# Optimization experiments

Hardware: AMD Instinct MI355X
Metric: run time of the kernel (lower is better)

Reference implementation:

```python
import jax, jax.numpy as jnp
import numpy as np


def setup_inputs() -> dict:
    key = jax.random.key(0)
    k1, k2, k3 = jax.random.split(key, 3)
    B, N, D = 8, 4096, 64
    q = jax.random.normal(k1, (B, N, D), dtype=jnp.float32)
    k = jax.random.normal(k2, (B, N, D), dtype=jnp.float32)
    v = jax.random.normal(k3, (B, N, D), dtype=jnp.float32)
    attn_mask = jnp.ones((B, N), dtype=jnp.int32)  # 1 = attend, 0 = padding
    return {"q": q, "k": k, "v": v, "attn_mask": attn_mask}


def reference(q, k, v, attn_mask):
    # q: [B, n_q, d], k/v: [B, n_k, d], attn_mask: [B, n_k]
    d = q.shape[-1]
    n_q, n_k = q.shape[1], k.shape[1]
    scale = jnp.sqrt(jnp.asarray(d, dtype=q.dtype))
    # [B, n_q, n_k] attention logits
    logits = jnp.einsum("bqd,bkd->bqk", q, k) / scale
    # causal (mask_future=True): tril keep-mask over (n_q, n_k)
    causal = jnp.tril(jnp.ones((n_q, n_k), dtype=bool))
    neg_inf = jnp.asarray(-jnp.inf, dtype=logits.dtype)
    logits = jnp.where(causal[None, :, :], logits, neg_inf)
    # padding mask broadcast over query dim: [B, 1, n_k]
    logits = jnp.where(attn_mask[:, None, :] == 0, neg_inf, logits)
    w = jax.nn.softmax(logits, axis=-1)
    return jnp.einsum("bqk,bkd->bqd", w, v)
```

## Files before the change

### kernel.cpp

```cpp
#include <hip/hip_runtime.h>


#define BATCH 8
#define SEQ   4096
#define DIM   64
#define QT    64
#define NKT   (SEQ / 64)

typedef __attribute__((ext_vector_type(8))) short bf16x8;
typedef __attribute__((ext_vector_type(4))) float f32x4;

__device__ inline short f2bf(float f) {
    unsigned u = __builtin_bit_cast(unsigned, f);
    u += 0x7FFFu + ((u >> 16) & 1u);
    return (short)(u >> 16);
}

__device__ inline unsigned pk2bf(float a, float b) {
    unsigned ua = __builtin_bit_cast(unsigned, a) + 0x8000u;
    unsigned ub = __builtin_bit_cast(unsigned, b) + 0x8000u;
    return __builtin_amdgcn_perm(ub, ua, 0x07060302u);
}

__device__ inline float fast_exp2(float x) {
#if __has_builtin(__builtin_amdgcn_exp2f)
    return __builtin_amdgcn_exp2f(x);
#else
    return exp2f(x);
#endif
}

__device__ inline void gl_lds16(const void* g, void* l) {
    __builtin_amdgcn_global_load_lds(
        (const __attribute__((address_space(1))) void*)g,
        (__attribute__((address_space(3))) void*)l, 16, 0, 0);
}

__global__ __launch_bounds__(256)
void prep_kv(const float* __restrict__ kg, const float* __restrict__ vg,
             const int* __restrict__ mg, short* __restrict__ kw,
             short* __restrict__ vw, float* __restrict__ mf) {
    const int tile = blockIdx.x;
    const float* kp = kg + (size_t)tile * 64 * DIM;
    const float* vp = vg + (size_t)tile * 64 * DIM;
    short* ko = kw + (size_t)tile * 4096;
    short* vo = vw + (size_t)tile * 4096;
    const int t = threadIdx.x;
    if (mf && t < 64) {
        const int* mp = mg + (size_t)tile * 64;
        mf[(size_t)tile * 64 + t] = mp[t] ? 0.0f : -1e30f;
    }
#pragma unroll
    for (int i = 0; i < 4; ++i) {
        const int flat = i * 256 + t;
        const int key = flat >> 4, d0 = (flat & 15) * 4;
        const float4 kv = *(const float4*)(kp + (size_t)key * DIM + d0);
        uint2 kpk;
        kpk.x = pk2bf(kv.x, kv.y); kpk.y = pk2bf(kv.z, kv.w);
        *(uint2*)(ko + (((d0 >> 3) << 6) + key) * 8 + (d0 & 7)) = kpk;
        const float4 vv = *(const float4*)(vp + (size_t)key * DIM + d0);
        const int kc = key >> 3, jk = key & 7;
        vo[((kc << 6) + d0 + 0) * 8 + jk] = f2bf(vv.x);
        vo[((kc << 6) + d0 + 1) * 8 + jk] = f2bf(vv.y);
        vo[((kc << 6) + d0 + 2) * 8 + jk] = f2bf(vv.z);
        vo[((kc << 6) + d0 + 3) * 8 + jk] = f2bf(vv.w);
    }
}

__global__ __launch_bounds__(512, 6)
void attn_split3(const float* __restrict__ qg, float* __restrict__ og,
                 const short* __restrict__ kw, const short* __restrict__ vw,
                 const float* __restrict__ mf, float* __restrict__ opart,
                 float* __restrict__ lpart) {
    __shared__ __align__(16) char smem[43008];
    short* KbS = (short*)smem;
    short* VbS = (short*)(smem + 16384);
    short* PbS = (short*)(smem + 32768);
    float* OX = (float*)smem;
    float* LB = (float*)(smem + 16384);

    const int t    = threadIdx.x;
    const int w    = t >> 6;
    const int L    = t & 63;
    const int c15  = L & 15;
    const int quad = L >> 4;
    const int qsub = w & 3;
    const int kh   = w >> 2;

    const int id  = blockIdx.x;
    const int b   = id & 7;
    const int r_  = id >> 3;
    const int j   = r_ & 31;
    const int ch  = r_ >> 5;
    const int nL  = 64 - j;
    const int qLt = 63 - j;

    const float* qp  = qg + (size_t)b * SEQ * DIM;
    const float* mb  = mf + (size_t)b * SEQ;
    const short* kwb = kw + (size_t)b * NKT * 4096;
    const short* vwb = vw + (size_t)b * NKT * 4096;
    float* osl = opart + (size_t)(b * 32 + j) * 8192;
    float* lsl = lpart + (size_t)(b * 32 + j) * 256;
    const float qscale = 0.125f * 1.44269504088896340736f;

    auto stage = [&](int bs, int kt) {
        const short* ks = kwb + (size_t)kt * 4096;
        const short* vs = vwb + (size_t)kt * 4096;
        const int off = w << 9;
        gl_lds16(ks + off + (L << 3), KbS + bs * 4096 + off);
        gl_lds16(vs + off + (L << 3), VbS + bs * 4096 + off);
    };

    short* Pw = PbS + w * 640;

    int sqt[2], sk0[2], sk1[2], smode[2], sos[2], sls[2], nseg;
    sos[0] = sos[1] = 0; sls[0] = sls[1] = 0;
    if (ch == 0) {
        nseg = 1;
        sqt[0] = qLt; sk0[0] = 0;  sk1[0] = 22; smode[0] = 0; sls[0] = 0;
    } else if (ch == 1) {
        if (nL >= 44) {
            nseg = 1;
            sqt[0] = qLt; sk0[0] = 22; sk1[0] = 44; smode[0] = 1; sos[0] = 0; sls[0] = 1;
        } else {
            nseg = 2;
            sqt[0] = qLt; sk0[0] = 22; sk1[0] = nL;      smode[0] = 1; sos[0] = 0; sls[0] = 1;
            sqt[1] = j;   sk0[1] = 0;  sk1[1] = 44 - nL; smode[1] = 0; sls[1] = 3;
        }
    } else {
        if (nL > 44) {
            nseg = 2;
            sqt[0] = qLt; sk0[0] = 44; sk1[0] = nL;    smode[0] = 1; sos[0] = 1; sls[0] = 2;
            sqt[1] = j;   sk0[1] = 0;  sk1[1] = j + 1; smode[1] = 2;
        } else if (nL == 44) {
            nseg = 1;
            sqt[0] = j; sk0[0] = 0; sk1[0] = j + 1; smode[0] = 2;
        } else {
            nseg = 1;
            sqt[0] = j; sk0[0] = 44 - nL; sk1[0] = j + 1; smode[0] = 1; sos[0] = 1; sls[0] = 2;
        }
    }

    for (int seg = 0; seg < nseg; ++seg) {
        const int qt   = sqt[seg];
        const int kt0  = sk0[seg];
        const int kt1  = sk1[seg];
        const int mode = smode[seg];

        const int qbase = qt * QT;
        const int qrow  = qbase + qsub * 16 + c15;

        bf16x8 Qf[2];
#pragma unroll
        for (int c = 0; c < 2; ++c) {
            const float* src = qp + (size_t)qrow * DIM + c * 32 + quad * 8;
            float4 x = *(const float4*)(src);
            float4 y = *(const float4*)(src + 4);
            bf16x8 f;
            f[0] = f2bf(x.x * qscale); f[1] = f2bf(x.y * qscale);
            f[2] = f2bf(x.z * qscale); f[3] = f2bf(x.w * qscale);
            f[4] = f2bf(y.x * qscale); f[5] = f2bf(y.y * qscale);
            f[6] = f2bf(y.z * qscale); f[7] = f2bf(y.w * qscale);
            Qf[c] = f;
        }

        float lsum = 0.0f;
        f32x4 Oacc[4];
#pragma unroll
        for (int nb = 0; nb < 4; ++nb) Oacc[nb] = (f32x4){0.f, 0.f, 0.f, 0.f};

        stage(0, kt0);

        for (int kt = kt0; kt < kt1; ++kt) {
            const int cur = (kt - kt0) & 1;
            __syncthreads();
            if (kt + 1 < kt1) stage(cur ^ 1, kt + 1);

            const short* Kt = KbS + cur * 4096;
            const short* Vt = VbS + cur * 4096;

            f32x4 sacc[2];
            sacc[0] = (f32x4){0.f, 0.f, 0.f, 0.f};
            sacc[1] = (f32x4){0.f, 0.f, 0.f, 0.f};
#pragma unroll
            for (int c = 0; c < 2; ++c) {
#pragma unroll
                for (int i = 0; i < 2; ++i) {
                    bf16x8 kf = *(const bf16x8*)&Kt[(((quad + 4 * c) << 6) + (2 * kh + i) * 16 + c15) * 8];
                    sacc[i] = __builtin_amdgcn_mfma_f32_16x16x32_bf16(kf, Qf[c], sacc[i], 0, 0, 0);
                }
            }

            const bool diag = (kt == qt);
#pragma unroll
            for (int i = 0; i < 2; ++i) {
                const int kb = 2 * kh + i;
                const float4 ma = *(const float4*)&mb[kt * 64 + kb * 16 + quad * 4];
                const float mar[4] = {ma.x, ma.y, ma.z, ma.w};
                float p[4];
#pragma unroll
                for (int r = 0; r < 4; ++r) {
                    float s = sacc[i][r] + mar[r];
                    if (diag) {
                        const int keyg = kt * 64 + kb * 16 + quad * 4 + r;
                        if (keyg > qrow) s = -1e30f;
                    }
                    p[r] = fast_exp2(fminf(s, 80.0f));
                    lsum += p[r];
                }
                uint2 pp;
                pp.x = pk2bf(p[0], p[1]);
                pp.y = pk2bf(p[2], p[3]);
                *(uint2*)&Pw[c15 * 40 + i * 16 + quad * 4] = pp;
            }

            bf16x8 pf = *(const bf16x8*)&Pw[c15 * 40 + quad * 8];
#pragma unroll
            for (int nb = 0; nb < 4; ++nb) {
                bf16x8 vf = *(const bf16x8*)&Vt[(((kh * 4 + quad) << 6) + nb * 16 + c15) * 8];
                Oacc[nb] = __builtin_amdgcn_mfma_f32_16x16x32_bf16(pf, vf, Oacc[nb], 0, 0, 0);
            }
        }

        lsum += __shfl_xor(lsum, 16);
        lsum += __shfl_xor(lsum, 32);

        __syncthreads();
        if (w >= 4) {
            const int g = w & 3;
#pragma unroll
            for (int r = 0; r < 4; ++r) {
                const int q = quad * 4 + r;
#pragma unroll
                for (int nb = 0; nb < 4; ++nb)
                    OX[(g * 16 + q) * 64 + nb * 16 + c15] = Oacc[nb][r];
            }
            if (quad == 0) LB[g * 16 + c15] = lsum;
        }
        __syncthreads();
        if (w < 4) {
            const float ltot = lsum + LB[w * 16 + c15];
            const float inv  = 1.0f / ltot;
            float* dst = (mode == 1) ? osl + (size_t)sos[seg] * 4096
                                     : og + ((size_t)b * SEQ + qbase) * DIM;
            if (mode != 2 && L < 16)
                lsl[sls[seg] * 64 + w * 16 + L] = ltot;
#pragma unroll
            for (int r = 0; r < 4; ++r) {
                const float ir = (mode == 2)
                    ? __shfl(inv, (L & 48) + ((L & 48) >> 2) + r) : 1.0f;
                const int rl = w * 16 + quad * 4 + r;
#pragma unroll
                for (int nb = 0; nb < 4; ++nb)
                    dst[(size_t)rl * DIM + nb * 16 + c15] =
                        (Oacc[nb][r] + OX[rl * 64 + nb * 16 + c15]) * ir;
            }
        }
        __syncthreads();
    }
}

__global__ __launch_bounds__(256)
void merge3(float* __restrict__ og, const float* __restrict__ opart,
            const float* __restrict__ lpart) {
    const int id = blockIdx.x;
    const int b = id & 7, j = id >> 3;
    const int nL = 64 - j, qLt = 63 - j;
    const float* os = opart + (size_t)(b * 32 + j) * 8192;
    const float* ls = lpart + (size_t)(b * 32 + j) * 256;
    const int t = threadIdx.x;
    const bool hasC = (nL > 44);

    float* opL = og + ((size_t)b * SEQ + (size_t)qLt * 64) * DIM;
#pragma unroll
    for (int i = 0; i < 4; ++i) {
        const int flat = i * 256 + t;
        const int row = flat >> 4;
        const int c4  = (flat & 15) * 4;
        float l = ls[row] + ls[64 + row];
        if (hasC) l += ls[128 + row];
        const float inv = 1.0f / l;
        const float4 a  = *(const float4*)(opL + (size_t)row * DIM + c4);
        const float4 p0 = *(const float4*)(os + (size_t)row * 64 + c4);
        float4 r;
        if (hasC) {
            const float4 p1 = *(const float4*)(os + 4096 + (size_t)row * 64 + c4);
            r.x = (a.x + p0.x + p1.x) * inv;
            r.y = (a.y + p0.y + p1.y) * inv;
            r.z = (a.z + p0.z + p1.z) * inv;
            r.w = (a.w + p0.w + p1.w) * inv;
        } else {
            r.x = (a.x + p0.x) * inv;
            r.y = (a.y + p0.y) * inv;
            r.z = (a.z + p0.z) * inv;
            r.w = (a.w + p0.w) * inv;
        }
        *(float4*)(opL + (size_t)row * DIM + c4) = r;
    }

    if (nL < 44) {
        float* opS = og + ((size_t)b * SEQ + (size_t)j * 64) * DIM;
#pragma unroll
        for (int i = 0; i < 4; ++i) {
            const int flat = i * 256 + t;
            const int row = flat >> 4;
            const int c4  = (flat & 15) * 4;
            const float inv = 1.0f / (ls[192 + row] + ls[128 + row]);
            const float4 a  = *(const float4*)(opS + (size_t)row * DIM + c4);
            const float4 p1 = *(const float4*)(os + 4096 + (size_t)row * 64 + c4);
            float4 r;
            r.x = (a.x + p1.x) * inv;
            r.y = (a.y + p1.y) * inv;
            r.z = (a.z + p1.z) * inv;
            r.w = (a.w + p1.w) * inv;
            *(float4*)(opS + (size_t)row * DIM + c4) = r;
        }
    }
}

template <bool WS>
__global__ __launch_bounds__(512, 4)
void attn_fwd(const float* __restrict__ qg, const float* __restrict__ kg,
              const float* __restrict__ vg, const int* __restrict__ mg,
              float* __restrict__ og, const short* __restrict__ kw,
              const short* __restrict__ vw) {
    __shared__ __align__(16) char smem[59392];
    short* KbS = (short*)smem;
    short* VbS = (short*)(smem + 16384);
    short* PbS = (short*)(smem + 32768);
    float* Ml  = (float*)(smem + 43008);
    float* OX = (float*)smem;
    float* LB = (float*)(smem + 16384);

    const int t    = threadIdx.x;
    const int w    = t >> 6;
    const int L    = t & 63;
    const int c15  = L & 15;
    const int quad = L >> 4;
    const int qsub = w & 3;
    const int kh   = w >> 2;

    const int id = blockIdx.x;
    const int b  = id & 7;
    const int j  = id >> 3;
    const int qb = (j < 32) ? (63 - j) : (j - 32);
    const int qbase  = qb * QT;
    const int ntiles = qb + 1;

    const float* qp = qg + (size_t)b * SEQ * DIM;
    const float* kp = kg + (size_t)b * SEQ * DIM;
    const float* vp = vg + (size_t)b * SEQ * DIM;
    const int*   mp = mg + (size_t)b * SEQ;
    const short* kwb = WS ? kw + (size_t)b * NKT * 4096 : nullptr;
    const short* vwb = WS ? vw + (size_t)b * NKT * 4096 : nullptr;

    const int qrow = qbase + qsub * 16 + c15;
    const float qscale = 0.125f * 1.44269504088896340736f;

    bf16x8 Qf[2];
#pragma unroll
    for (int c = 0; c < 2; ++c) {
        const float* src = qp + (size_t)qrow * DIM + c * 32 + quad * 8;
        float4 x = *(const float4*)(src);
        float4 y = *(const float4*)(src + 4);
        bf16x8 f;
        f[0] = f2bf(x.x * qscale); f[1] = f2bf(x.y * qscale);
        f[2] = f2bf(x.z * qscale); f[3] = f2bf(x.w * qscale);
        f[4] = f2bf(y.x * qscale); f[5] = f2bf(y.y * qscale);
        f[6] = f2bf(y.z * qscale); f[7] = f2bf(y.w * qscale);
        Qf[c] = f;
    }

    auto stage = [&](int bs, int kt) {
        const short* ks = kwb + (size_t)kt * 4096;
        const short* vs = vwb + (size_t)kt * 4096;
        const int off = w << 9;
        gl_lds16(ks + off + (L << 3), KbS + bs * 4096 + off);
        gl_lds16(vs + off + (L << 3), VbS + bs * 4096 + off);
    };

    for (int i = t; i < ntiles * 64; i += 512)
        Ml[i] = mp[i] ? 0.0f : -1e30f;

    float lsum = 0.0f;
    f32x4 Oacc[4];
#pragma unroll
    for (int nb = 0; nb < 4; ++nb) Oacc[nb] = (f32x4){0.f, 0.f, 0.f, 0.f};

    if constexpr (WS) stage(0, 0);

    short* Pw = PbS + w * 640;

    for (int kt = 0; kt < ntiles; ++kt) {
        const int cur = WS ? (kt & 1) : 0;

        if constexpr (!WS) {
            __syncthreads();
#pragma unroll
            for (int it = 0; it < 2; ++it) {
                const int flat = it * 512 + t;
                const int key = flat >> 4, d0 = (flat & 15) * 4;
                const float4 kv = *(const float4*)(kp + (size_t)(kt * 64 + key) * DIM + d0);
                uint2 kk;
                kk.x = pk2bf(kv.x, kv.y); kk.y = pk2bf(kv.z, kv.w);
                *(uint2*)&KbS[(((d0 >> 3) << 6) + key) * 8 + (d0 & 7)] = kk;
                const float4 vv = *(const float4*)(vp + (size_t)(kt * 64 + key) * DIM + d0);
                const int kc = key >> 3, jk = key & 7;
                VbS[((kc << 6) + d0 + 0) * 8 + jk] = f2bf(vv.x);
                VbS[((kc << 6) + d0 + 1) * 8 + jk] = f2bf(vv.y);
                VbS[((kc << 6) + d0 + 2) * 8 + jk] = f2bf(vv.z);
                VbS[((kc << 6) + d0 + 3) * 8 + jk] = f2bf(vv.w);
            }
            __syncthreads();
        } else {
            __syncthreads();
            if (kt + 1 < ntiles) stage(cur ^ 1, kt + 1);
        }

        const short* Kt = KbS + cur * 4096;
        const short* Vt = VbS + cur * 4096;

        f32x4 sacc[2];
        sacc[0] = (f32x4){0.f, 0.f, 0.f, 0.f};
        sacc[1] = (f32x4){0.f, 0.f, 0.f, 0.f};
#pragma unroll
        for (int c = 0; c < 2; ++c) {
#pragma unroll
            for (int i = 0; i < 2; ++i) {
                bf16x8 kf = *(const bf16x8*)&Kt[(((quad + 4 * c) << 6) + (2 * kh + i) * 16 + c15) * 8];
                sacc[i] = __builtin_amdgcn_mfma_f32_16x16x32_bf16(kf, Qf[c], sacc[i], 0, 0, 0);
            }
        }

        const bool diag = (kt == ntiles - 1);
#pragma unroll
        for (int i = 0; i < 2; ++i) {
            const int kb = 2 * kh + i;
            const float4 ma = *(const float4*)&Ml[kt * 64 + kb * 16 + quad * 4];
            const float mar[4] = {ma.x, ma.y, ma.z, ma.w};
            float p[4];
#pragma unroll
            for (int r = 0; r < 4; ++r) {
                float s = sacc[i][r] + mar[r];
                if (diag) {
                    const int keyg = kt * 64 + kb * 16 + quad * 4 + r;
                    if (keyg > qrow) s = -1e30f;
                }
                p[r] = fast_exp2(fminf(s, 80.0f));
                lsum += p[r];
            }
            uint2 pp;
            pp.x = pk2bf(p[0], p[1]);
            pp.y = pk2bf(p[2], p[3]);
            *(uint2*)&Pw[c15 * 40 + i * 16 + quad * 4] = pp;
        }

        bf16x8 pf = *(const bf16x8*)&Pw[c15 * 40 + quad * 8];
#pragma unroll
        for (int nb = 0; nb < 4; ++nb) {
            bf16x8 vf = *(const bf16x8*)&Vt[(((kh * 4 + quad) << 6) + nb * 16 + c15) * 8];
            Oacc[nb] = __builtin_amdgcn_mfma_f32_16x16x32_bf16(pf, vf, Oacc[nb], 0, 0, 0);
        }
    }

    lsum += __shfl_xor(lsum, 16);
    lsum += __shfl_xor(lsum, 32);

    __syncthreads();
    if (w >= 4) {
        const int g = w & 3;
#pragma unroll
        for (int r = 0; r < 4; ++r) {
            const int q = quad * 4 + r;
#pragma unroll
            for (int nb = 0; nb < 4; ++nb)
                OX[(g * 16 + q) * 64 + nb * 16 + c15] = Oacc[nb][r];
        }
        if (quad == 0) LB[g * 16 + c15] = lsum;
    }
    __syncthreads();
    if (w < 4) {
        const float inv = 1.0f / (lsum + LB[w * 16 + c15]);
        float* op = og + (size_t)b * SEQ * DIM;
#pragma unroll
        for (int r = 0; r < 4; ++r) {
            const float ir = __shfl(inv, (L & 48) + ((L & 48) >> 2) + r);
            const int row = qbase + w * 16 + quad * 4 + r;
#pragma unroll
            for (int nb = 0; nb < 4; ++nb)
                op[(size_t)row * DIM + nb * 16 + c15] =
                    (Oacc[nb][r] + OX[(w * 16 + quad * 4 + r) * 64 + nb * 16 + c15]) * ir;
        }
    }
}

extern "C" void kernel_launch(void* const* d_in, const int* in_sizes, int n_in,
                              void* d_out, int out_size, void* d_ws, size_t ws_size,
                              hipStream_t stream) {
    (void)in_sizes; (void)n_in; (void)out_size;
    const float* q = (const float*)d_in[0];
    const float* k = (const float*)d_in[1];
    const float* v = (const float*)d_in[2];
    const int*   m = (const int*)d_in[3];
    float* o = (float*)d_out;

    const size_t kvB    = (size_t)BATCH * NKT * 4096 * sizeof(short);
    const size_t maddB  = (size_t)BATCH * SEQ * sizeof(float);
    const size_t opartB = (size_t)BATCH * 32 * 8192 * sizeof(float);
    const size_t lpartB = (size_t)BATCH * 32 * 256 * sizeof(float);
    const size_t need3  = 2 * kvB + maddB + opartB + lpartB;

    if (ws_size >= need3) {
        short* kw = (short*)d_ws;
        short* vw = kw + (size_t)BATCH * NKT * 4096;
        float* mf = (float*)((char*)d_ws + 2 * kvB);
        float* opart = (float*)((char*)d_ws + 2 * kvB + maddB);
        float* lpart = opart + (size_t)BATCH * 32 * 8192;
        prep_kv<<<dim3(BATCH * NKT), 256, 0, stream>>>(k, v, m, kw, vw, mf);
        attn_split3<<<dim3(768), 512, 0, stream>>>(q, o, kw, vw, mf, opart, lpart);
        merge3<<<dim3(256), 256, 0, stream>>>(o, opart, lpart);
    } else if (ws_size >= 2 * kvB) {
        short* kw = (short*)d_ws;
        short* vw = kw + (size_t)BATCH * NKT * 4096;
        prep_kv<<<dim3(BATCH * NKT), 256, 0, stream>>>(k, v, m, kw, vw, nullptr);
        attn_fwd<true><<<dim3(512), 512, 0, stream>>>(q, k, v, m, o, kw, vw);
    } else {
        attn_fwd<false><<<dim3(512), 512, 0, stream>>>(q, k, v, m, o, nullptr, nullptr);
    }
}
```

Before: 124.0 us.

## Split causal attention into four chunks and keep P in registers

Result: slower. 131.3 us (+5.9%).

```diff
diff --git a/kernel.cpp b/kernel.cpp
--- a/kernel.cpp
+++ b/kernel.cpp
@@ -9,6 +9,7 @@
 
 typedef __attribute__((ext_vector_type(8))) short bf16x8;
 typedef __attribute__((ext_vector_type(4))) float f32x4;
+typedef __attribute__((ext_vector_type(4))) unsigned u32x4;
 
 __device__ inline short f2bf(float f) {
     unsigned u = __builtin_bit_cast(unsigned, f);
@@ -59,23 +60,23 @@
         kpk.x = pk2bf(kv.x, kv.y); kpk.y = pk2bf(kv.z, kv.w);
         *(uint2*)(ko + (((d0 >> 3) << 6) + key) * 8 + (d0 & 7)) = kpk;
         const float4 vv = *(const float4*)(vp + (size_t)key * DIM + d0);
-        const int kc = key >> 3, jk = key & 7;
-        vo[((kc << 6) + d0 + 0) * 8 + jk] = f2bf(vv.x);
-        vo[((kc << 6) + d0 + 1) * 8 + jk] = f2bf(vv.y);
-        vo[((kc << 6) + d0 + 2) * 8 + jk] = f2bf(vv.z);
-        vo[((kc << 6) + d0 + 3) * 8 + jk] = f2bf(vv.w);
-    }
-}
-
-__global__ __launch_bounds__(512, 6)
-void attn_split3(const float* __restrict__ qg, float* __restrict__ og,
+        const int vcell = ((key >> 5) << 2) | ((key >> 2) & 3);
+        const int vj    = (((key >> 4) & 1) << 2) | (key & 3);
+        vo[((vcell << 6) + d0 + 0) * 8 + vj] = f2bf(vv.x);
+        vo[((vcell << 6) + d0 + 1) * 8 + vj] = f2bf(vv.y);
+        vo[((vcell << 6) + d0 + 2) * 8 + vj] = f2bf(vv.z);
+        vo[((vcell << 6) + d0 + 3) * 8 + vj] = f2bf(vv.w);
+    }
+}
+
+__global__ __launch_bounds__(512, 8)
+void attn_split4(const float* __restrict__ qg, float* __restrict__ og,
                  const short* __restrict__ kw, const short* __restrict__ vw,
                  const float* __restrict__ mf, float* __restrict__ opart,
                  float* __restrict__ lpart) {
-    __shared__ __align__(16) char smem[43008];
+    __shared__ __align__(16) char smem[32768];
     short* KbS = (short*)smem;
     short* VbS = (short*)(smem + 16384);
-    short* PbS = (short*)(smem + 32768);
     float* OX = (float*)smem;
     float* LB = (float*)(smem + 16384);
 
@@ -99,8 +100,8 @@
     const float* mb  = mf + (size_t)b * SEQ;
     const short* kwb = kw + (size_t)b * NKT * 4096;
     const short* vwb = vw + (size_t)b * NKT * 4096;
-    float* osl = opart + (size_t)(b * 32 + j) * 8192;
-    float* lsl = lpart + (size_t)(b * 32 + j) * 256;
+    float* osl = opart + (size_t)(b * 32 + j) * 12288;
+    float* lsl = lpart + (size_t)(b * 32 + j) * 384;
     const float qscale = 0.125f * 1.44269504088896340736f;
 
     auto stage = [&](int bs, int kt) {
@@ -111,33 +112,34 @@
         gl_lds16(vs + off + (L << 3), VbS + bs * 4096 + off);
     };
 
-    short* Pw = PbS + w * 640;
-
     int sqt[2], sk0[2], sk1[2], smode[2], sos[2], sls[2], nseg;
     sos[0] = sos[1] = 0; sls[0] = sls[1] = 0;
     if (ch == 0) {
         nseg = 1;
-        sqt[0] = qLt; sk0[0] = 0;  sk1[0] = 22; smode[0] = 0; sls[0] = 0;
+        sqt[0] = qLt; sk0[0] = 0;  sk1[0] = 16; smode[0] = 0; sls[0] = 0;
     } else if (ch == 1) {
-        if (nL >= 44) {
+        nseg = 1;
+        sqt[0] = qLt; sk0[0] = 16; sk1[0] = 32; smode[0] = 1; sos[0] = 0; sls[0] = 1;
+    } else if (ch == 2) {
+        if (nL >= 48) {
             nseg = 1;
-            sqt[0] = qLt; sk0[0] = 22; sk1[0] = 44; smode[0] = 1; sos[0] = 0; sls[0] = 1;
+            sqt[0] = qLt; sk0[0] = 32; sk1[0] = 48; smode[0] = 1; sos[0] = 1; sls[0] = 2;
         } else {
             nseg = 2;
-            sqt[0] = qLt; sk0[0] = 22; sk1[0] = nL;      smode[0] = 1; sos[0] = 0; sls[0] = 1;
-            sqt[1] = j;   sk0[1] = 0;  sk1[1] = 44 - nL; smode[1] = 0; sls[1] = 3;
+            sqt[0] = qLt; sk0[0] = 32; sk1[0] = nL;      smode[0] = 1; sos[0] = 1; sls[0] = 2;
+            sqt[1] = j;   sk0[1] = 0;  sk1[1] = 48 - nL; smode[1] = 0; sls[1] = 4;
         }
     } else {
-        if (nL > 44) {
+        if (nL > 48) {
             nseg = 2;
-            sqt[0] = qLt; sk0[0] = 44; sk1[0] = nL;    smode[0] = 1; sos[0] = 1; sls[0] = 2;
+            sqt[0] = qLt; sk0[0] = 48; sk1[0] = nL;    smode[0] = 1; sos[0] = 2; sls[0] = 3;
             sqt[1] = j;   sk0[1] = 0;  sk1[1] = j + 1; smode[1] = 2;
-        } else if (nL == 44) {
+        } else if (nL == 48) {
             nseg = 1;
             sqt[0] = j; sk0[0] = 0; sk1[0] = j + 1; smode[0] = 2;
         } else {
             nseg = 1;
-            sqt[0] = j; sk0[0] = 44 - nL; sk1[0] = j + 1; smode[0] = 1; sos[0] = 1; sls[0] = 2;
+            sqt[0] = j; sk0[0] = 48 - nL; sk1[0] = j + 1; smode[0] = 1; sos[0] = 2; sls[0] = 5;
         }
     }
 
@@ -192,6 +194,7 @@
             }
 
             const bool diag = (kt == qt);
+            unsigned pu[4];
 #pragma unroll
             for (int i = 0; i < 2; ++i) {
                 const int kb = 2 * kh + i;
@@ -208,13 +211,12 @@
                     p[r] = fast_exp2(fminf(s, 80.0f));
                     lsum += p[r];
                 }
-                uint2 pp;
-                pp.x = pk2bf(p[0], p[1]);
-                pp.y = pk2bf(p[2], p[3]);
-                *(uint2*)&Pw[c15 * 40 + i * 16 + quad * 4] = pp;
-            }
-
-            bf16x8 pf = *(const bf16x8*)&Pw[c15 * 40 + quad * 8];
+                pu[2 * i]     = pk2bf(p[0], p[1]);
+                pu[2 * i + 1] = pk2bf(p[2], p[3]);
+            }
+
+            const bf16x8 pf = __builtin_bit_cast(bf16x8,
+                (u32x4){pu[0], pu[1], pu[2], pu[3]});
 #pragma unroll
             for (int nb = 0; nb < 4; ++nb) {
                 bf16x8 vf = *(const bf16x8*)&Vt[(((kh * 4 + quad) << 6) + nb * 16 + c15) * 8];
@@ -261,15 +263,15 @@
 }
 
 __global__ __launch_bounds__(256)
-void merge3(float* __restrict__ og, const float* __restrict__ opart,
+void merge4(float* __restrict__ og, const float* __restrict__ opart,
             const float* __restrict__ lpart) {
     const int id = blockIdx.x;
     const int b = id & 7, j = id >> 3;
     const int nL = 64 - j, qLt = 63 - j;
-    const float* os = opart + (size_t)(b * 32 + j) * 8192;
-    const float* ls = lpart + (size_t)(b * 32 + j) * 256;
+    const float* os = opart + (size_t)(b * 32 + j) * 12288;
+    const float* ls = lpart + (size_t)(b * 32 + j) * 384;
     const int t = threadIdx.x;
-    const bool hasC = (nL > 44);
+    const bool has3 = (nL > 48);
 
     float* opL = og + ((size_t)b * SEQ + (size_t)qLt * 64) * DIM;
 #pragma unroll
@@ -277,42 +279,40 @@
         const int flat = i * 256 + t;
         const int row = flat >> 4;
         const int c4  = (flat & 15) * 4;
-        float l = ls[row] + ls[64 + row];
-        if (hasC) l += ls[128 + row];
+        float l = ls[row] + ls[64 + row] + ls[128 + row];
+        if (has3) l += ls[192 + row];
         const float inv = 1.0f / l;
         const float4 a  = *(const float4*)(opL + (size_t)row * DIM + c4);
         const float4 p0 = *(const float4*)(os + (size_t)row * 64 + c4);
+        const float4 p1 = *(const float4*)(os + 4096 + (size_t)row * 64 + c4);
+        float sx = a.x + p0.x + p1.x;
+        float sy = a.y + p0.y + p1.y;
+        float sz = a.z + p0.z + p1.z;
+        float sw = a.w + p0.w + p1.w;
+        if (has3) {
+            const float4 p2 = *(const float4*)(os + 8192 + (size_t)row * 64 + c4);
+            sx += p2.x; sy += p2.y; sz += p2.z; sw += p2.w;
+        }
         float4 r;
-        if (hasC) {
-            const float4 p1 = *(const float4*)(os + 4096 + (size_t)row * 64 + c4);
-            r.x = (a.x + p0.x + p1.x) * inv;
-            r.y = (a.y + p0.y + p1.y) * inv;
-            r.z = (a.z + p0.z + p1.z) * inv;
-            r.w = (a.w + p0.w + p1.w) * inv;
-        } else {
-            r.x = (a.x + p0.x) * inv;
-            r.y = (a.y + p0.y) * inv;
-            r.z = (a.z + p0.z) * inv;
-            r.w = (a.w + p0.w) * inv;
-        }
+        r.x = sx * inv; r.y = sy * inv; r.z = sz * inv; r.w = sw * inv;
         *(float4*)(opL + (size_t)row * DIM + c4) = r;
     }
 
-    if (nL < 44) {
+    if (nL < 48) {
         float* opS = og + ((size_t)b * SEQ + (size_t)j * 64) * DIM;
 #pragma unroll
         for (int i = 0; i < 4; ++i) {
             const int flat = i * 256 + t;
             const int row = flat >> 4;
             const int c4  = (flat & 15) * 4;
-            const float inv = 1.0f / (ls[192 + row] + ls[128 + row]);
+            const float inv = 1.0f / (ls[256 + row] + ls[320 + row]);
             const float4 a  = *(const float4*)(opS + (size_t)row * DIM + c4);
-            const float4 p1 = *(const float4*)(os + 4096 + (size_t)row * 64 + c4);
+            const float4 p2 = *(const float4*)(os + 8192 + (size_t)row * 64 + c4);
             float4 r;
-            r.x = (a.x + p1.x) * inv;
-            r.y = (a.y + p1.y) * inv;
-            r.z = (a.z + p1.z) * inv;
-            r.w = (a.w + p1.w) * inv;
+            r.x = (a.x + p2.x) * inv;
+            r.y = (a.y + p2.y) * inv;
+            r.z = (a.z + p2.z) * inv;
+            r.w = (a.w + p2.w) * inv;
             *(float4*)(opS + (size_t)row * DIM + c4) = r;
         }
     }
@@ -327,7 +327,6 @@
     __shared__ __align__(16) char smem[59392];
     short* KbS = (short*)smem;
     short* VbS = (short*)(smem + 16384);
-    short* PbS = (short*)(smem + 32768);
     float* Ml  = (float*)(smem + 43008);
     float* OX = (float*)smem;
     float* LB = (float*)(smem + 16384);
@@ -389,8 +388,6 @@
 
     if constexpr (WS) stage(0, 0);
 
-    short* Pw = PbS + w * 640;
-
     for (int kt = 0; kt < ntiles; ++kt) {
         const int cur = WS ? (kt & 1) : 0;
 
@@ -405,11 +402,12 @@
                 kk.x = pk2bf(kv.x, kv.y); kk.y = pk2bf(kv.z, kv.w);
                 *(uint2*)&KbS[(((d0 >> 3) << 6) + key) * 8 + (d0 & 7)] = kk;
                 const float4 vv = *(const float4*)(vp + (size_t)(kt * 64 + key) * DIM + d0);
-                const int kc = key >> 3, jk = key & 7;
-                VbS[((kc << 6) + d0 + 0) * 8 + jk] = f2bf(vv.x);
-                VbS[((kc << 6) + d0 + 1) * 8 + jk] = f2bf(vv.y);
-                VbS[((kc << 6) + d0 + 2) * 8 + jk] = f2bf(vv.z);
-                VbS[((kc << 6) + d0 + 3) * 8 + jk] = f2bf(vv.w);
+                const int vcell = ((key >> 5) << 2) | ((key >> 2) & 3);
+                const int vj    = (((key >> 4) & 1) << 2) | (key & 3);
+                VbS[((vcell << 6) + d0 + 0) * 8 + vj] = f2bf(vv.x);
+                VbS[((vcell << 6) + d0 + 1) * 8 + vj] = f2bf(vv.y);
+                VbS[((vcell << 6) + d0 + 2) * 8 + vj] = f2bf(vv.z);
+                VbS[((vcell << 6) + d0 + 3) * 8 + vj] = f2bf(vv.w);
             }
             __syncthreads();
         } else {
@@ -433,6 +431,7 @@
         }
 
         const bool diag = (kt == ntiles - 1);
+        unsigned pu[4];
 #pragma unroll
         for (int i = 0; i < 2; ++i) {
             const int kb = 2 * kh + i;
@@ -449,13 +448,12 @@
                 p[r] = fast_exp2(fminf(s, 80.0f));
                 lsum += p[r];
             }
-            uint2 pp;
-            pp.x = pk2bf(p[0], p[1]);
-            pp.y = pk2bf(p[2], p[3]);
-            *(uint2*)&Pw[c15 * 40 + i * 16 + quad * 4] = pp;
-        }
-
-        bf16x8 pf = *(const bf16x8*)&Pw[c15 * 40 + quad * 8];
+            pu[2 * i]     = pk2bf(p[0], p[1]);
+            pu[2 * i + 1] = pk2bf(p[2], p[3]);
+        }
+
+        const bf16x8 pf = __builtin_bit_cast(bf16x8,
+            (u32x4){pu[0], pu[1], pu[2], pu[3]});
 #pragma unroll
         for (int nb = 0; nb < 4; ++nb) {
             bf16x8 vf = *(const bf16x8*)&Vt[(((kh * 4 + quad) << 6) + nb * 16 + c15) * 8];
@@ -506,19 +504,19 @@
 
     const size_t kvB    = (size_t)BATCH * NKT * 4096 * sizeof(short);
     const size_t maddB  = (size_t)BATCH * SEQ * sizeof(float);
-    const size_t opartB = (size_t)BATCH * 32 * 8192 * sizeof(float);
-    const size_t lpartB = (size_t)BATCH * 32 * 256 * sizeof(float);
-    const size_t need3  = 2 * kvB + maddB + opartB + lpartB;
-
-    if (ws_size >= need3) {
+    const size_t opartB = (size_t)BATCH * 32 * 12288 * sizeof(float);
+    const size_t lpartB = (size_t)BATCH * 32 * 384 * sizeof(float);
+    const size_t need4  = 2 * kvB + maddB + opartB + lpartB;
+
+    if (ws_size >= need4) {
         short* kw = (short*)d_ws;
         short* vw = kw + (size_t)BATCH * NKT * 4096;
         float* mf = (float*)((char*)d_ws + 2 * kvB);
         float* opart = (float*)((char*)d_ws + 2 * kvB + maddB);
-        float* lpart = opart + (size_t)BATCH * 32 * 8192;
+        float* lpart = opart + (size_t)BATCH * 32 * 12288;
         prep_kv<<<dim3(BATCH * NKT), 256, 0, stream>>>(k, v, m, kw, vw, mf);
-        attn_split3<<<dim3(768), 512, 0, stream>>>(q, o, kw, vw, mf, opart, lpart);
-        merge3<<<dim3(256), 256, 0, stream>>>(o, opart, lpart);
+        attn_split4<<<dim3(1024), 512, 0, stream>>>(q, o, kw, vw, mf, opart, lpart);
+        merge4<<<dim3(256), 256, 0, stream>>>(o, opart, lpart);
     } else if (ws_size >= 2 * kvB) {
         short* kw = (short*)d_ws;
         short* vw = kw + (size_t)BATCH * NKT * 4096;
```

## Keep softmax probabilities in registers by permuting V layout to match MFMA output

Applied to the files above, without the earlier changes.

New measurement: 124.9 us. Within noise of the previous version (+0.8%).

```diff
diff --git a/kernel.cpp b/kernel.cpp
--- a/kernel.cpp
+++ b/kernel.cpp
@@ -9,6 +9,7 @@
 
 typedef __attribute__((ext_vector_type(8))) short bf16x8;
 typedef __attribute__((ext_vector_type(4))) float f32x4;
+typedef __attribute__((ext_vector_type(4))) unsigned u32x4;
 
 __device__ inline short f2bf(float f) {
     unsigned u = __builtin_bit_cast(unsigned, f);
@@ -59,11 +60,12 @@
         kpk.x = pk2bf(kv.x, kv.y); kpk.y = pk2bf(kv.z, kv.w);
         *(uint2*)(ko + (((d0 >> 3) << 6) + key) * 8 + (d0 & 7)) = kpk;
         const float4 vv = *(const float4*)(vp + (size_t)key * DIM + d0);
-        const int kc = key >> 3, jk = key & 7;
-        vo[((kc << 6) + d0 + 0) * 8 + jk] = f2bf(vv.x);
-        vo[((kc << 6) + d0 + 1) * 8 + jk] = f2bf(vv.y);
-        vo[((kc << 6) + d0 + 2) * 8 + jk] = f2bf(vv.z);
-        vo[((kc << 6) + d0 + 3) * 8 + jk] = f2bf(vv.w);
+        const int vcell = ((key >> 5) << 2) | ((key >> 2) & 3);
+        const int vj    = (((key >> 4) & 1) << 2) | (key & 3);
+        vo[((vcell << 6) + d0 + 0) * 8 + vj] = f2bf(vv.x);
+        vo[((vcell << 6) + d0 + 1) * 8 + vj] = f2bf(vv.y);
+        vo[((vcell << 6) + d0 + 2) * 8 + vj] = f2bf(vv.z);
+        vo[((vcell << 6) + d0 + 3) * 8 + vj] = f2bf(vv.w);
     }
 }
 
@@ -72,10 +74,9 @@
                  const short* __restrict__ kw, const short* __restrict__ vw,
                  const float* __restrict__ mf, float* __restrict__ opart,
                  float* __restrict__ lpart) {
-    __shared__ __align__(16) char smem[43008];
+    __shared__ __align__(16) char smem[32768];
     short* KbS = (short*)smem;
     short* VbS = (short*)(smem + 16384);
-    short* PbS = (short*)(smem + 32768);
     float* OX = (float*)smem;
     float* LB = (float*)(smem + 16384);
 
@@ -110,8 +111,6 @@
         gl_lds16(ks + off + (L << 3), KbS + bs * 4096 + off);
         gl_lds16(vs + off + (L << 3), VbS + bs * 4096 + off);
     };
-
-    short* Pw = PbS + w * 640;
 
     int sqt[2], sk0[2], sk1[2], smode[2], sos[2], sls[2], nseg;
     sos[0] = sos[1] = 0; sls[0] = sls[1] = 0;
@@ -179,6 +178,9 @@
             const short* Kt = KbS + cur * 4096;
             const short* Vt = VbS + cur * 4096;
 
+            const float4 ma0 = *(const float4*)&mb[kt * 64 + (2 * kh + 0) * 16 + quad * 4];
+            const float4 ma1 = *(const float4*)&mb[kt * 64 + (2 * kh + 1) * 16 + quad * 4];
+
             f32x4 sacc[2];
             sacc[0] = (f32x4){0.f, 0.f, 0.f, 0.f};
             sacc[1] = (f32x4){0.f, 0.f, 0.f, 0.f};
@@ -192,10 +194,11 @@
             }
 
             const bool diag = (kt == qt);
+            unsigned pu[4];
 #pragma unroll
             for (int i = 0; i < 2; ++i) {
                 const int kb = 2 * kh + i;
-                const float4 ma = *(const float4*)&mb[kt * 64 + kb * 16 + quad * 4];
+                const float4 ma = i ? ma1 : ma0;
                 const float mar[4] = {ma.x, ma.y, ma.z, ma.w};
                 float p[4];
 #pragma unroll
@@ -208,13 +211,12 @@
                     p[r] = fast_exp2(fminf(s, 80.0f));
                     lsum += p[r];
                 }
-                uint2 pp;
-                pp.x = pk2bf(p[0], p[1]);
-                pp.y = pk2bf(p[2], p[3]);
-                *(uint2*)&Pw[c15 * 40 + i * 16 + quad * 4] = pp;
-            }
-
-            bf16x8 pf = *(const bf16x8*)&Pw[c15 * 40 + quad * 8];
+                pu[2 * i]     = pk2bf(p[0], p[1]);
+                pu[2 * i + 1] = pk2bf(p[2], p[3]);
+            }
+
+            const bf16x8 pf = __builtin_bit_cast(bf16x8,
+                (u32x4){pu[0], pu[1], pu[2], pu[3]});
 #pragma unroll
             for (int nb = 0; nb < 4; ++nb) {
                 bf16x8 vf = *(const bf16x8*)&Vt[(((kh * 4 + quad) << 6) + nb * 16 + c15) * 8];
@@ -327,7 +329,6 @@
     __shared__ __align__(16) char smem[59392];
     short* KbS = (short*)smem;
     short* VbS = (short*)(smem + 16384);
-    short* PbS = (short*)(smem + 32768);
     float* Ml  = (float*)(smem + 43008);
     float* OX = (float*)smem;
     float* LB = (float*)(smem + 16384);
@@ -389,8 +390,6 @@
 
     if constexpr (WS) stage(0, 0);
 
-    short* Pw = PbS + w * 640;
-
     for (int kt = 0; kt < ntiles; ++kt) {
         const int cur = WS ? (kt & 1) : 0;
 
@@ -405,11 +404,12 @@
                 kk.x = pk2bf(kv.x, kv.y); kk.y = pk2bf(kv.z, kv.w);
                 *(uint2*)&KbS[(((d0 >> 3) << 6) + key) * 8 + (d0 & 7)] = kk;
                 const float4 vv = *(const float4*)(vp + (size_t)(kt * 64 + key) * DIM + d0);
-                const int kc = key >> 3, jk = key & 7;
-                VbS[((kc << 6) + d0 + 0) * 8 + jk] = f2bf(vv.x);
-                VbS[((kc << 6) + d0 + 1) * 8 + jk] = f2bf(vv.y);
-                VbS[((kc << 6) + d0 + 2) * 8 + jk] = f2bf(vv.z);
-                VbS[((kc << 6) + d0 + 3) * 8 + jk] = f2bf(vv.w);
+                const int vcell = ((key >> 5) << 2) | ((key >> 2) & 3);
+                const int vj    = (((key >> 4) & 1) << 2) | (key & 3);
+                VbS[((vcell << 6) + d0 + 0) * 8 + vj] = f2bf(vv.x);
+                VbS[((vcell << 6) + d0 + 1) * 8 + vj] = f2bf(vv.y);
+                VbS[((vcell << 6) + d0 + 2) * 8 + vj] = f2bf(vv.z);
+                VbS[((vcell << 6) + d0 + 3) * 8 + vj] = f2bf(vv.w);
             }
             __syncthreads();
         } else {
@@ -433,6 +433,7 @@
         }
 
         const bool diag = (kt == ntiles - 1);
+        unsigned pu[4];
 #pragma unroll
         for (int i = 0; i < 2; ++i) {
             const int kb = 2 * kh + i;
@@ -449,13 +450,12 @@
                 p[r] = fast_exp2(fminf(s, 80.0f));
                 lsum += p[r];
             }
-            uint2 pp;
-            pp.x = pk2bf(p[0], p[1]);
-            pp.y = pk2bf(p[2], p[3]);
-            *(uint2*)&Pw[c15 * 40 + i * 16 + quad * 4] = pp;
-        }
-
-        bf16x8 pf = *(const bf16x8*)&Pw[c15 * 40 + quad * 8];
+            pu[2 * i]     = pk2bf(p[0], p[1]);
+            pu[2 * i + 1] = pk2bf(p[2], p[3]);
+        }
+
+        const bf16x8 pf = __builtin_bit_cast(bf16x8,
+            (u32x4){pu[0], pu[1], pu[2], pu[3]});
 #pragma unroll
         for (int nb = 0; nb < 4; ++nb) {
             bf16x8 vf = *(const bf16x8*)&Vt[(((kh * 4 + quad) << 6) + nb * 16 + c15) * 8];
```
